# Optimization experiments

Measured on AMD Instinct MI355X. Metric: run time of the kernel, lower is better.

## Reference

```python
import jax, jax.numpy as jnp
import numpy as np

T, B, D = 256, 16, 512          # time, batch, intermediate_dim (GRU is seq-first)
HR = 256                         # router_dim
EXPERT_DIMS = [0, 128, 256, 512]
NUM_TASKS = 4
COST_EXP = 1.0
BN_EPS = 1e-5


def _gru(x, w_ih, w_hh, b_ih, b_hh):
    """PyTorch-semantics GRU over axis 0. x: (T, ..., D) -> (T, ..., H).
    Works batched (T,B,D) or unbatched (N,D) exactly like nn.GRU."""
    H = w_hh.shape[1]
    gi = x @ w_ih.T + b_ih            # (T, ..., 3H) input projections, done once
    h0 = jnp.zeros(x.shape[1:-1] + (H,), x.dtype)

    def step(h, gi_t):
        gh = h @ w_hh.T + b_hh
        i_r, i_z, i_n = jnp.split(gi_t, 3, axis=-1)
        h_r, h_z, h_n = jnp.split(gh, 3, axis=-1)
        r = jax.nn.sigmoid(i_r + h_r)
        z = jax.nn.sigmoid(i_z + h_z)
        n = jnp.tanh(i_n + r * h_n)
        h_new = (1.0 - z) * n + z * h
        return h_new, h_new

    _, ys = jax.lax.scan(step, h0, gi)
    return ys


def setup_inputs() -> dict:
    key = jax.random.key(0)
    ks = iter(jax.random.split(key, 64))

    def p(shape, fan_in):
        return (jax.random.normal(next(ks), shape, jnp.float32) / np.sqrt(fan_in)).astype(jnp.float32)

    inp = {
        'x': jax.random.normal(next(ks), (T, B, D), jnp.float32),
        'task_ids': jax.random.randint(next(ks), (T, B), 0, NUM_TASKS),
        # router params
        'router_w_ih': p((3 * HR, D), D),
        'router_w_hh': p((3 * HR, HR), HR),
        'router_b_ih': jnp.zeros((3 * HR,), jnp.float32),
        'router_b_hh': jnp.zeros((3 * HR,), jnp.float32),
        'router_out_w': p((len(EXPERT_DIMS), HR), HR),
        'router_out_b': jnp.zeros((len(EXPERT_DIMS),), jnp.float32),
    }
    for i, H in enumerate(EXPERT_DIMS):
        if H == 0:
            continue
        inp[f'e{i}_w_ih'] = p((3 * H, D), D)
        inp[f'e{i}_w_hh'] = p((3 * H, H), H)
        inp[f'e{i}_b_ih'] = jnp.zeros((3 * H,), jnp.float32)
        inp[f'e{i}_b_hh'] = jnp.zeros((3 * H,), jnp.float32)
        inp[f'e{i}_bn_g'] = jnp.ones((H,), jnp.float32)
        inp[f'e{i}_bn_b'] = jnp.zeros((H,), jnp.float32)
        inp[f'e{i}_out_w'] = p((D, H), H)
        inp[f'e{i}_out_b'] = jnp.zeros((D,), jnp.float32)
    return inp


def reference(x, task_ids,
              router_w_ih, router_w_hh, router_b_ih, router_b_hh,
              router_out_w, router_out_b,
              e1_w_ih, e1_w_hh, e1_b_ih, e1_b_hh, e1_bn_g, e1_bn_b, e1_out_w, e1_out_b,
              e2_w_ih, e2_w_hh, e2_b_ih, e2_b_hh, e2_bn_g, e2_bn_b, e2_out_w, e2_out_b,
              e3_w_ih, e3_w_hh, e3_b_ih, e3_b_hh, e3_bn_g, e3_bn_b, e3_out_w, e3_out_b):
    E = len(EXPERT_DIMS)
    # ---- router: GRU -> ReLU -> Linear -> softmax ----
    hs = _gru(x, router_w_ih, router_w_hh, router_b_ih, router_b_hh)   # (T,B,HR)
    logits = jax.nn.relu(hs) @ router_out_w.T + router_out_b           # (T,B,E)
    raw = jax.nn.softmax(logits, axis=-1)                              # raw_router_output
    # no dropout configured -> router_output == raw, all experts active

    # ---- task expert usage losses ----
    costs = jnp.asarray([d ** COST_EXP for d in EXPERT_DIMS], logits.dtype)
    eul = jnp.einsum('tbe,e->tb', raw, costs).reshape(-1)
    tflat = task_ids.reshape(-1)
    sums = jax.ops.segment_sum(eul, tflat, num_segments=NUM_TASKS)
    cnts = jax.ops.segment_sum(jnp.ones_like(eul), tflat, num_segments=NUM_TASKS)
    task_losses = sums / cnts                                           # (NUM_TASKS,)

    # ---- experts: each sees the flat (N,D) tokens as ONE unbatched GRU sequence ----
    flat_x = x.reshape(-1, D)                                           # (N,D)
    gates = raw.reshape(-1, E)                                          # (N,E)
    out = gates[:, 0:1] * flat_x                                        # expert 0 = identity

    eps = [(e1_w_ih, e1_w_hh, e1_b_ih, e1_b_hh, e1_bn_g, e1_bn_b, e1_out_w, e1_out_b),
           (e2_w_ih, e2_w_hh, e2_b_ih, e2_b_hh, e2_bn_g, e2_bn_b, e2_out_w, e2_out_b),
           (e3_w_ih, e3_w_hh, e3_b_ih, e3_b_hh, e3_bn_g, e3_bn_b, e3_out_w, e3_out_b)]
    for i, (w_ih, w_hh, b_ih, b_hh, g, b, ow, ob) in enumerate(eps, start=1):
        h = _gru(flat_x, w_ih, w_hh, b_ih, b_hh)                        # (N,H) unbatched seq
        mu = h.mean(0)
        var = ((h - mu) ** 2).mean(0)                                   # biased var (train-mode BN)
        hn = (h - mu) / jnp.sqrt(var + BN_EPS) * g + b
        eo = jax.nn.relu(hn) @ ow.T + ob                                # (N,D)
        out = out + gates[:, i:i + 1] * eo

    final_output = out.reshape(T, B, D)
    return final_output, raw, task_losses
```

## Files before the change

kernel.cpp:

```cpp
#include <hip/hip_runtime.h>
#include <math.h>

constexpr int TT = 256, BB = 16, DD = 512;
constexpr int NTOK = 4096;
constexpr int RTOT = 3456;
constexpr int E1OFF = 768, E2OFF = 1152, E3OFF = 1920;

constexpr size_t OFF_TSUM = 0;
constexpr size_t OFF_TCNT = 16;
constexpr size_t OFF_CNT  = 32;
constexpr size_t ZBYTES   = 64;
constexpr size_t OFF_GI   = 4096;
constexpr size_t OFF_HS   = OFF_GI  + (size_t)NTOK*RTOT*4;
constexpr size_t OFF_HA3  = OFF_HS  + (size_t)NTOK*256*4;
constexpr size_t OFF_HA2  = OFF_HA3 + (size_t)NTOK*512*4;
constexpr size_t OFF_HA1  = OFF_HA2 + (size_t)NTOK*256*4;
constexpr size_t OFF_AP   = OFF_HA1 + (size_t)NTOK*128*4;
constexpr size_t OFF_MU   = OFF_AP  + (size_t)NTOK*896*4;
constexpr size_t OFF_RSTD = OFF_MU  + 896*4;
constexpr size_t POISON_BYTES = (size_t)NTOK*(256+512+256+128)*4;

__device__ __forceinline__ bool is_poison(float v) {
  return __float_as_uint(v) == 0xAAAAAAAAu;
}

__global__ __launch_bounds__(256) void gemm1_kernel(
    const float* __restrict__ X,
    const float* __restrict__ wR, const float* __restrict__ w1,
    const float* __restrict__ w2, const float* __restrict__ w3,
    const float* __restrict__ bR, const float* __restrict__ b1,
    const float* __restrict__ b2, const float* __restrict__ b3,
    float* __restrict__ GI)
{
  __shared__ float At[32*64];
  __shared__ float Bt[32*64];
  const int n0 = blockIdx.x * 64;
  const int r0 = blockIdx.y * 64;
  const float* W; const float* bias; int rs;
  if (r0 < 768)       { W = wR; bias = bR; rs = 0; }
  else if (r0 < 1152) { W = w1; bias = b1; rs = 768; }
  else if (r0 < 1920) { W = w2; bias = b2; rs = 1152; }
  else                { W = w3; bias = b3; rs = 1920; }
  const int lr0 = r0 - rs;
  const int tid = threadIdx.x;
  const int lm = tid & 63, lk4 = tid >> 6;
  const int tx = tid & 15, ty = tid >> 4;
  float acc[4][4];
#pragma unroll
  for (int i = 0; i < 4; ++i)
#pragma unroll
    for (int q = 0; q < 4; ++q) acc[i][q] = 0.f;

  for (int kb = 0; kb < 512; kb += 32) {
    const float4 a0 = *(const float4*)(X + (size_t)(n0+lm)*512 + kb + lk4*8);
    const float4 a1 = *(const float4*)(X + (size_t)(n0+lm)*512 + kb + lk4*8 + 4);
    const float4 c0 = *(const float4*)(W + (size_t)(lr0+lm)*512 + kb + lk4*8);
    const float4 c1 = *(const float4*)(W + (size_t)(lr0+lm)*512 + kb + lk4*8 + 4);
    __syncthreads();
    At[(lk4*8+0)*64+lm]=a0.x; At[(lk4*8+1)*64+lm]=a0.y; At[(lk4*8+2)*64+lm]=a0.z; At[(lk4*8+3)*64+lm]=a0.w;
    At[(lk4*8+4)*64+lm]=a1.x; At[(lk4*8+5)*64+lm]=a1.y; At[(lk4*8+6)*64+lm]=a1.z; At[(lk4*8+7)*64+lm]=a1.w;
    Bt[(lk4*8+0)*64+lm]=c0.x; Bt[(lk4*8+1)*64+lm]=c0.y; Bt[(lk4*8+2)*64+lm]=c0.z; Bt[(lk4*8+3)*64+lm]=c0.w;
    Bt[(lk4*8+4)*64+lm]=c1.x; Bt[(lk4*8+5)*64+lm]=c1.y; Bt[(lk4*8+6)*64+lm]=c1.z; Bt[(lk4*8+7)*64+lm]=c1.w;
    __syncthreads();
#pragma unroll
    for (int k = 0; k < 32; ++k) {
      const float4 av = *(const float4*)&At[k*64 + ty*4];
      const float4 bv = *(const float4*)&Bt[k*64 + tx*4];
      acc[0][0]=fmaf(av.x,bv.x,acc[0][0]); acc[0][1]=fmaf(av.x,bv.y,acc[0][1]); acc[0][2]=fmaf(av.x,bv.z,acc[0][2]); acc[0][3]=fmaf(av.x,bv.w,acc[0][3]);
      acc[1][0]=fmaf(av.y,bv.x,acc[1][0]); acc[1][1]=fmaf(av.y,bv.y,acc[1][1]); acc[1][2]=fmaf(av.y,bv.z,acc[1][2]); acc[1][3]=fmaf(av.y,bv.w,acc[1][3]);
      acc[2][0]=fmaf(av.z,bv.x,acc[2][0]); acc[2][1]=fmaf(av.z,bv.y,acc[2][1]); acc[2][2]=fmaf(av.z,bv.z,acc[2][2]); acc[2][3]=fmaf(av.z,bv.w,acc[2][3]);
      acc[3][0]=fmaf(av.w,bv.x,acc[3][0]); acc[3][1]=fmaf(av.w,bv.y,acc[3][1]); acc[3][2]=fmaf(av.w,bv.z,acc[3][2]); acc[3][3]=fmaf(av.w,bv.w,acc[3][3]);
    }
  }
  const float4 bb = *(const float4*)(bias + lr0 + tx*4);
#pragma unroll
  for (int i = 0; i < 4; ++i) {
    float4 o;
    o.x = acc[i][0] + bb.x; o.y = acc[i][1] + bb.y; o.z = acc[i][2] + bb.z; o.w = acc[i][3] + bb.w;
    *(float4*)(GI + (size_t)(n0+ty*4+i)*RTOT + r0 + tx*4) = o;
  }
}

struct ScanArgs {
  const float* GI;
  const float* rwhh; const float* rbhh; float* hs;
  const float* w1; const float* b1; float* ha1;
  const float* w2; const float* b2; float* ha2;
  const float* w3; const float* b3; float* ha3;
  int* cnt;
};

template<int H, int OPW>
__device__ void expert_scan(const float* __restrict__ GIe, const float* __restrict__ whh,
                            const float* __restrict__ bhh, float* __restrict__ hall,
                            float* __restrict__ sm, int wg)
{
  constexpr int KCN = 512 / OPW;
  constexpr int CHUNK = H / KCN;
  constexpr int NF4 = CHUNK / 4;
  const int tid = threadIdx.x;
  const int j = tid / KCN, kc = tid % KCN;
  const int jg = wg * OPW + j;

  float4 wr[NF4], wz[NF4], wn[NF4];
#pragma unroll
  for (int i4 = 0; i4 < NF4; ++i4) {
    const int kk = kc * CHUNK + ((i4 + kc) & (NF4 - 1)) * 4;
    wr[i4] = *(const float4*)(whh + (size_t)jg * H + kk);
    wz[i4] = *(const float4*)(whh + (size_t)(H + jg) * H + kk);
    wn[i4] = *(const float4*)(whh + (size_t)(2*H + jg) * H + kk);
  }
  float gbr = 0.f, gbz = 0.f, gbn = 0.f;
  float gr0 = 0.f, gz0 = 0.f, gn0 = 0.f, gr1 = 0.f, gz1 = 0.f, gn1 = 0.f;
  if (kc == 0) {
    gbr = bhh[jg]; gbz = bhh[H + jg]; gbn = bhh[2*H + jg];
    gr0 = GIe[jg]; gz0 = GIe[H + jg]; gn0 = GIe[2*H + jg];
    const float* g1 = GIe + RTOT;
    gr1 = g1[jg]; gz1 = g1[H + jg]; gn1 = g1[2*H + jg];
  }
  for (int t = 0; t < NTOK; ++t) {
    float val = 0.f;
    if (tid < H && t > 0) {
      const volatile float* p = (const volatile float*)(hall + (size_t)(t - 1) * H + tid);
      val = *p;
      while (is_poison(val)) val = *p;
    }
    __syncthreads();
    if (tid < H) sm[tid] = val;
    __syncthreads();
    float gr2 = 0.f, gz2 = 0.f, gn2 = 0.f;
    if (kc == 0 && t + 2 < NTOK) {
      const float* g = GIe + (size_t)(t + 2) * RTOT;
      gr2 = g[jg]; gz2 = g[H + jg]; gn2 = g[2*H + jg];
    }
    float pr = 0.f, pz = 0.f, pn = 0.f;
#pragma unroll
    for (int i4 = 0; i4 < NF4; ++i4) {
      const float4 h4 = *(const float4*)(sm + kc * CHUNK + ((i4 + kc) & (NF4 - 1)) * 4);
      pr = fmaf(wr[i4].x, h4.x, pr); pr = fmaf(wr[i4].y, h4.y, pr);
      pr = fmaf(wr[i4].z, h4.z, pr); pr = fmaf(wr[i4].w, h4.w, pr);
      pz = fmaf(wz[i4].x, h4.x, pz); pz = fmaf(wz[i4].y, h4.y, pz);
      pz = fmaf(wz[i4].z, h4.z, pz); pz = fmaf(wz[i4].w, h4.w, pz);
      pn = fmaf(wn[i4].x, h4.x, pn); pn = fmaf(wn[i4].y, h4.y, pn);
      pn = fmaf(wn[i4].z, h4.z, pn); pn = fmaf(wn[i4].w, h4.w, pn);
    }
#pragma unroll
    for (int off = KCN / 2; off; off >>= 1) {
      pr += __shfl_down(pr, off); pz += __shfl_down(pz, off); pn += __shfl_down(pn, off);
    }
    if (kc == 0) {
      const float hprev = sm[jg];
      const float rg = 1.f / (1.f + expf(-(gr0 + gbr + pr)));
      const float zg = 1.f / (1.f + expf(-(gz0 + gbz + pz)));
      const float nn = tanhf(gn0 + rg * (pn + gbn));
      const float hn = (1.f - zg) * nn + zg * hprev;
      *(volatile float*)(hall + (size_t)t * H + jg) = hn;
    }
    gr0 = gr1; gz0 = gz1; gn0 = gn1;
    gr1 = gr2; gz1 = gz2; gn1 = gn2;
  }
}

__device__ void router_scan(const float* __restrict__ GI, const float* __restrict__ whh,
                            const float* __restrict__ bhh, float* __restrict__ hs,
                            float* __restrict__ sm, int wg)
{
  float* hsmB = sm;
  float* pbuf = sm + 16 * 260;
  const int tid = threadIdx.x;
  const int j = tid >> 4, kc = tid & 15;
  const int jg = wg * 32 + j;
  float4 wr4[4], wz4[4], wn4[4];
#pragma unroll
  for (int i4 = 0; i4 < 4; ++i4) {
    const int kk = kc * 16 + ((i4 + kc) & 3) * 4;
    wr4[i4] = *(const float4*)(whh + (size_t)jg * 256 + kk);
    wz4[i4] = *(const float4*)(whh + (size_t)(256 + jg) * 256 + kk);
    wn4[i4] = *(const float4*)(whh + (size_t)(512 + jg) * 256 + kk);
  }
  const int b2 = tid >> 5, j2 = tid & 31;
  const int jg2 = wg * 32 + j2;
  const float gbr = bhh[jg2], gbz = bhh[256 + jg2], gbn = bhh[512 + jg2];
  float gr0, gz0, gn0, gr1, gz1, gn1;
  { const float* g = GI + (size_t)b2 * RTOT;        gr0 = g[jg2]; gz0 = g[256 + jg2]; gn0 = g[512 + jg2]; }
  { const float* g = GI + (size_t)(16 + b2) * RTOT; gr1 = g[jg2]; gz1 = g[256 + jg2]; gn1 = g[512 + jg2]; }
  const int pb = tid >> 5, pk = (tid & 31) * 8;

  for (int t = 0; t < TT; ++t) {
    float gr2 = 0.f, gz2 = 0.f, gn2 = 0.f;
    if (t + 2 < TT) {
      const float* g = GI + (size_t)((t + 2) * 16 + b2) * RTOT;
      gr2 = g[jg2]; gz2 = g[256 + jg2]; gn2 = g[512 + jg2];
    }
    float v[8];
    if (t == 0) {
#pragma unroll
      for (int u = 0; u < 8; ++u) v[u] = 0.f;
    } else {
      const volatile float* q = (const volatile float*)(hs + (size_t)(t - 1) * 4096 + tid * 8);
#pragma unroll
      for (int u = 0; u < 8; ++u) v[u] = q[u];
      bool bad = true;
      while (bad) {
        bad = false;
#pragma unroll
        for (int u = 0; u < 8; ++u)
          if (is_poison(v[u])) { v[u] = q[u]; bad = true; }
      }
    }
    __syncthreads();
    *(float4*)(hsmB + pb * 260 + pk)     = make_float4(v[0], v[1], v[2], v[3]);
    *(float4*)(hsmB + pb * 260 + pk + 4) = make_float4(v[4], v[5], v[6], v[7]);
    __syncthreads();
    float ar[16], az[16], an[16];
#pragma unroll
    for (int b = 0; b < 16; ++b) { ar[b] = 0.f; az[b] = 0.f; an[b] = 0.f; }
#pragma unroll
    for (int i4 = 0; i4 < 4; ++i4) {
      const int col = kc * 16 + ((i4 + kc) & 3) * 4;
#pragma unroll
      for (int b = 0; b < 16; ++b) {
        const float4 h4 = *(const float4*)(hsmB + b * 260 + col);
        ar[b] = fmaf(wr4[i4].x, h4.x, ar[b]); ar[b] = fmaf(wr4[i4].y, h4.y, ar[b]);
        ar[b] = fmaf(wr4[i4].z, h4.z, ar[b]); ar[b] = fmaf(wr4[i4].w, h4.w, ar[b]);
        az[b] = fmaf(wz4[i4].x, h4.x, az[b]); az[b] = fmaf(wz4[i4].y, h4.y, az[b]);
        az[b] = fmaf(wz4[i4].z, h4.z, az[b]); az[b] = fmaf(wz4[i4].w, h4.w, az[b]);
        an[b] = fmaf(wn4[i4].x, h4.x, an[b]); an[b] = fmaf(wn4[i4].y, h4.y, an[b]);
        an[b] = fmaf(wn4[i4].w, h4.w, an[b]); an[b] = fmaf(wn4[i4].z, h4.z, an[b]);
      }
    }
#pragma unroll
    for (int off = 8; off; off >>= 1) {
#pragma unroll
      for (int b = 0; b < 16; ++b) {
        ar[b] += __shfl_down(ar[b], off);
        az[b] += __shfl_down(az[b], off);
        an[b] += __shfl_down(an[b], off);
      }
    }
    if (kc == 0) {
#pragma unroll
      for (int b = 0; b < 16; ++b) {
        pbuf[(b * 32 + j) * 3 + 0] = ar[b];
        pbuf[(b * 32 + j) * 3 + 1] = az[b];
        pbuf[(b * 32 + j) * 3 + 2] = an[b];
      }
    }
    __syncthreads();
    const float pr = pbuf[(b2 * 32 + j2) * 3 + 0];
    const float pz = pbuf[(b2 * 32 + j2) * 3 + 1];
    const float pn = pbuf[(b2 * 32 + j2) * 3 + 2];
    const float hprev = hsmB[b2 * 260 + jg2];
    const float rg = 1.f / (1.f + expf(-(gr0 + gbr + pr)));
    const float zg = 1.f / (1.f + expf(-(gz0 + gbz + pz)));
    const float nn = tanhf(gn0 + rg * (pn + gbn));
    const float hn = (1.f - zg) * nn + zg * hprev;
    *(volatile float*)(hs + (size_t)t * 4096 + b2 * 256 + jg2) = hn;
    gr0 = gr1; gz0 = gz1; gn0 = gn1;
    gr1 = gr2; gz1 = gz2; gn1 = gn2;
  }
}

__global__ __launch_bounds__(512, 1) void scan_kernel(ScanArgs A)
{
  __shared__ float sm[16 * 260 + 1536];
  __shared__ int role_s[2];
  if (threadIdx.x == 0) {
    unsigned x;
    asm volatile("s_getreg_b32 %0, hwreg(HW_REG_XCC_ID)" : "=s"(x));
    const int xcd = (int)(x & 7u);
    role_s[0] = xcd;
    role_s[1] = atomicAdd(A.cnt + xcd, 1);
  }
  __syncthreads();
  const int xcd = role_s[0], r = role_s[1];
  if (xcd == 0)      { if (r < 32) expert_scan<512, 16>(A.GI + E3OFF, A.w3, A.b3, A.ha3, sm, r); }
  else if (xcd == 1) { if (r < 8)  router_scan(A.GI, A.rwhh, A.rbhh, A.hs, sm, r); }
  else if (xcd == 2) { if (r < 16) expert_scan<256, 16>(A.GI + E2OFF, A.w2, A.b2, A.ha2, sm, r); }
  else if (xcd == 3) { if (r < 4)  expert_scan<128, 32>(A.GI + E1OFF, A.w1, A.b1, A.ha1, sm, r); }
}

__global__ __launch_bounds__(256) void router_out_kernel(
    const float* __restrict__ hs, const float* __restrict__ ow, const float* __restrict__ ob,
    const int* __restrict__ tids, float* __restrict__ raw_out,
    float* __restrict__ tsum, float* __restrict__ tcnt)
{
  const int tid = threadIdx.x;
  const int lane = tid & 63, w = tid >> 6;
  const int n = blockIdx.x * 4 + w;
  float s0 = 0.f, s1 = 0.f, s2 = 0.f, s3 = 0.f;
#pragma unroll
  for (int q = 0; q < 4; ++q) {
    const int jj = lane + q * 64;
    float h = hs[(size_t)n * 256 + jj];
    h = h > 0.f ? h : 0.f;
    s0 = fmaf(h, ow[jj], s0);
    s1 = fmaf(h, ow[256 + jj], s1);
    s2 = fmaf(h, ow[512 + jj], s2);
    s3 = fmaf(h, ow[768 + jj], s3);
  }
  for (int off = 32; off; off >>= 1) {
    s0 += __shfl_xor(s0, off); s1 += __shfl_xor(s1, off);
    s2 += __shfl_xor(s2, off); s3 += __shfl_xor(s3, off);
  }
  if (lane == 0) {
    const float l0 = s0 + ob[0], l1 = s1 + ob[1], l2 = s2 + ob[2], l3 = s3 + ob[3];
    const float m = fmaxf(fmaxf(l0, l1), fmaxf(l2, l3));
    const float e0 = expf(l0 - m), e1 = expf(l1 - m), e2 = expf(l2 - m), e3 = expf(l3 - m);
    const float inv = 1.f / (e0 + e1 + e2 + e3);
    float4 rv; rv.x = e0 * inv; rv.y = e1 * inv; rv.z = e2 * inv; rv.w = e3 * inv;
    *(float4*)(raw_out + (size_t)n * 4) = rv;
    const float eul = rv.y * 128.f + rv.z * 256.f + rv.w * 512.f;
    const int tk = tids[n];
    atomicAdd(&tsum[tk], eul);
    atomicAdd(&tcnt[tk], 1.f);
  }
}

__global__ __launch_bounds__(256) void bn_stats_kernel(
    const float* __restrict__ h1, const float* __restrict__ h2, const float* __restrict__ h3,
    float* __restrict__ mu, float* __restrict__ rstd)
{
  const int c = blockIdx.x;
  const float* hp; int He, hc;
  if (c < 128)      { hp = h1; He = 128; hc = c; }
  else if (c < 384) { hp = h2; He = 256; hc = c - 128; }
  else              { hp = h3; He = 512; hc = c - 384; }
  float s = 0.f, s2 = 0.f;
  for (int r = threadIdx.x; r < NTOK; r += 256) {
    const float v = hp[(size_t)r * He + hc];
    s += v; s2 = fmaf(v, v, s2);
  }
  for (int off = 32; off; off >>= 1) { s += __shfl_xor(s, off); s2 += __shfl_xor(s2, off); }
  __shared__ float red[8];
  const int lane = threadIdx.x & 63, w = threadIdx.x >> 6;
  if (lane == 0) { red[w] = s; red[4 + w] = s2; }
  __syncthreads();
  if (threadIdx.x == 0) {
    const float S = red[0] + red[1] + red[2] + red[3];
    const float S2 = red[4] + red[5] + red[6] + red[7];
    const float m = S * (1.f / 4096.f);
    float v = S2 * (1.f / 4096.f) - m * m;
    v = v > 0.f ? v : 0.f;
    mu[c] = m;
    rstd[c] = 1.f / sqrtf(v + 1e-5f);
  }
}

__global__ __launch_bounds__(256) void aprime_kernel(
    const float* __restrict__ h1, const float* __restrict__ h2, const float* __restrict__ h3,
    const float* __restrict__ g1, const float* __restrict__ be1,
    const float* __restrict__ g2, const float* __restrict__ be2,
    const float* __restrict__ g3, const float* __restrict__ be3,
    const float* __restrict__ mu, const float* __restrict__ rstd,
    const float* __restrict__ raw, float* __restrict__ Ap,
    const float* __restrict__ tsum, const float* __restrict__ tcnt, float* __restrict__ tl_out)
{
  if (blockIdx.x == 4096) {
    if (threadIdx.x < 4) tl_out[threadIdx.x] = tsum[threadIdx.x] / tcnt[threadIdx.x];
    return;
  }
  const int n = blockIdx.x;
  for (int c = threadIdx.x; c < 896; c += 256) {
    const float* hp; const float* gg; const float* bb; int He, hc, e;
    if (c < 128)      { hp = h1; gg = g1; bb = be1; He = 128; hc = c;       e = 1; }
    else if (c < 384) { hp = h2; gg = g2; bb = be2; He = 256; hc = c - 128; e = 2; }
    else              { hp = h3; gg = g3; bb = be3; He = 512; hc = c - 384; e = 3; }
    const float h = hp[(size_t)n * He + hc];
    float v = (h - mu[c]) * rstd[c] * gg[hc] + bb[hc];
    v = v > 0.f ? v : 0.f;
    Ap[(size_t)n * 896 + c] = raw[(size_t)n * 4 + e] * v;
  }
}

__global__ __launch_bounds__(256) void out_gemm_kernel(
    const float* __restrict__ Ap,
    const float* __restrict__ ow1, const float* __restrict__ ow2, const float* __restrict__ ow3,
    const float* __restrict__ ob1, const float* __restrict__ ob2, const float* __restrict__ ob3,
    const float* __restrict__ X, const float* __restrict__ raw, float* __restrict__ out)
{
  __shared__ float At[32*64];
  __shared__ float Bt[32*64];
  const int n0 = blockIdx.x * 64;
  const int d0 = blockIdx.y * 64;
  const int tid = threadIdx.x;
  const int lm = tid & 63, lk4 = tid >> 6;
  const int tx = tid & 15, ty = tid >> 4;
  float acc[4][4];
#pragma unroll
  for (int i = 0; i < 4; ++i)
#pragma unroll
    for (int q = 0; q < 4; ++q) acc[i][q] = 0.f;

  for (int kb = 0; kb < 896; kb += 32) {
    const float* W; int He, ko;
    if (kb < 128)      { W = ow1; He = 128; ko = 0; }
    else if (kb < 384) { W = ow2; He = 256; ko = 128; }
    else               { W = ow3; He = 512; ko = 384; }
    const float4 a0 = *(const float4*)(Ap + (size_t)(n0+lm)*896 + kb + lk4*8);
    const float4 a1 = *(const float4*)(Ap + (size_t)(n0+lm)*896 + kb + lk4*8 + 4);
    const float4 c0 = *(const float4*)(W + (size_t)(d0+lm)*He + (kb - ko) + lk4*8);
    const float4 c1 = *(const float4*)(W + (size_t)(d0+lm)*He + (kb - ko) + lk4*8 + 4);
    __syncthreads();
    At[(lk4*8+0)*64+lm]=a0.x; At[(lk4*8+1)*64+lm]=a0.y; At[(lk4*8+2)*64+lm]=a0.z; At[(lk4*8+3)*64+lm]=a0.w;
    At[(lk4*8+4)*64+lm]=a1.x; At[(lk4*8+5)*64+lm]=a1.y; At[(lk4*8+6)*64+lm]=a1.z; At[(lk4*8+7)*64+lm]=a1.w;
    Bt[(lk4*8+0)*64+lm]=c0.x; Bt[(lk4*8+1)*64+lm]=c0.y; Bt[(lk4*8+2)*64+lm]=c0.z; Bt[(lk4*8+3)*64+lm]=c0.w;
    Bt[(lk4*8+4)*64+lm]=c1.x; Bt[(lk4*8+5)*64+lm]=c1.y; Bt[(lk4*8+6)*64+lm]=c1.z; Bt[(lk4*8+7)*64+lm]=c1.w;
    __syncthreads();
#pragma unroll
    for (int k = 0; k < 32; ++k) {
      const float4 av = *(const float4*)&At[k*64 + ty*4];
      const float4 bv = *(const float4*)&Bt[k*64 + tx*4];
      acc[0][0]=fmaf(av.x,bv.x,acc[0][0]); acc[0][1]=fmaf(av.x,bv.y,acc[0][1]); acc[0][2]=fmaf(av.x,bv.z,acc[0][2]); acc[0][3]=fmaf(av.x,bv.w,acc[0][3]);
      acc[1][0]=fmaf(av.y,bv.x,acc[1][0]); acc[1][1]=fmaf(av.y,bv.y,acc[1][1]); acc[1][2]=fmaf(av.y,bv.z,acc[1][2]); acc[1][3]=fmaf(av.y,bv.w,acc[1][3]);
      acc[2][0]=fmaf(av.z,bv.x,acc[2][0]); acc[2][1]=fmaf(av.z,bv.y,acc[2][1]); acc[2][2]=fmaf(av.z,bv.z,acc[2][2]); acc[2][3]=fmaf(av.z,bv.w,acc[2][3]);
      acc[3][0]=fmaf(av.w,bv.x,acc[3][0]); acc[3][1]=fmaf(av.w,bv.y,acc[3][1]); acc[3][2]=fmaf(av.w,bv.z,acc[3][2]); acc[3][3]=fmaf(av.w,bv.w,acc[3][3]);
    }
  }
#pragma unroll
  for (int i = 0; i < 4; ++i) {
    const int n = n0 + ty * 4 + i;
    const float4 g  = *(const float4*)(raw + (size_t)n * 4);
    const float4 xv = *(const float4*)(X + (size_t)n * 512 + d0 + tx * 4);
    const float4 o1 = *(const float4*)(ob1 + d0 + tx * 4);
    const float4 o2 = *(const float4*)(ob2 + d0 + tx * 4);
    const float4 o3 = *(const float4*)(ob3 + d0 + tx * 4);
    float4 o;
    o.x = acc[i][0] + g.x*xv.x + g.y*o1.x + g.z*o2.x + g.w*o3.x;
    o.y = acc[i][1] + g.x*xv.y + g.y*o1.y + g.z*o2.y + g.w*o3.y;
    o.z = acc[i][2] + g.x*xv.z + g.y*o1.z + g.z*o2.z + g.w*o3.z;
    o.w = acc[i][3] + g.x*xv.w + g.y*o1.w + g.z*o2.w + g.w*o3.w;
    *(float4*)(out + (size_t)n * 512 + d0 + tx * 4) = o;
  }
}

extern "C" void kernel_launch(void* const* d_in, const int* in_sizes, int n_in,
                              void* d_out, int out_size, void* d_ws, size_t ws_size,
                              hipStream_t stream) {
  const float* x    = (const float*)d_in[0];
  const int*   tids = (const int*)d_in[1];
  const float* rwih = (const float*)d_in[2];
  const float* rwhh = (const float*)d_in[3];
  const float* rbih = (const float*)d_in[4];
  const float* rbhh = (const float*)d_in[5];
  const float* row  = (const float*)d_in[6];
  const float* rob  = (const float*)d_in[7];
  const float* w1ih = (const float*)d_in[8];
  const float* w1hh = (const float*)d_in[9];
  const float* b1ih = (const float*)d_in[10];
  const float* b1hh = (const float*)d_in[11];
  const float* bn1g = (const float*)d_in[12];
  const float* bn1b = (const float*)d_in[13];
  const float* ow1  = (const float*)d_in[14];
  const float* ob1  = (const float*)d_in[15];
  const float* w2ih = (const float*)d_in[16];
  const float* w2hh = (const float*)d_in[17];
  const float* b2ih = (const float*)d_in[18];
  const float* b2hh = (const float*)d_in[19];
  const float* bn2g = (const float*)d_in[20];
  const float* bn2b = (const float*)d_in[21];
  const float* ow2  = (const float*)d_in[22];
  const float* ob2  = (const float*)d_in[23];
  const float* w3ih = (const float*)d_in[24];
  const float* w3hh = (const float*)d_in[25];
  const float* b3ih = (const float*)d_in[26];
  const float* b3hh = (const float*)d_in[27];
  const float* bn3g = (const float*)d_in[28];
  const float* bn3b = (const float*)d_in[29];
  const float* ow3  = (const float*)d_in[30];
  const float* ob3  = (const float*)d_in[31];

  char* ws = (char*)d_ws;
  float* tsum = (float*)(ws + OFF_TSUM);
  float* tcnt = (float*)(ws + OFF_TCNT);
  int*   cnt  = (int*)(ws + OFF_CNT);
  float* GI   = (float*)(ws + OFF_GI);
  float* hs   = (float*)(ws + OFF_HS);
  float* ha3  = (float*)(ws + OFF_HA3);
  float* ha2  = (float*)(ws + OFF_HA2);
  float* ha1  = (float*)(ws + OFF_HA1);
  float* Ap   = (float*)(ws + OFF_AP);
  float* mu   = (float*)(ws + OFF_MU);
  float* rstd = (float*)(ws + OFF_RSTD);

  float* outp = (float*)d_out;
  float* rawp = outp + (size_t)NTOK * DD;
  float* tlp  = rawp + (size_t)NTOK * 4;

  hipMemsetAsync(ws, 0, ZBYTES, stream);
  hipMemsetAsync(ws + OFF_HS, 0xAA, POISON_BYTES, stream);

  gemm1_kernel<<<dim3(64, 54), 256, 0, stream>>>(x, rwih, w1ih, w2ih, w3ih,
                                                 rbih, b1ih, b2ih, b3ih, GI);

  ScanArgs sa;
  sa.GI = GI; sa.rwhh = rwhh; sa.rbhh = rbhh; sa.hs = hs;
  sa.w1 = w1hh; sa.b1 = b1hh; sa.ha1 = ha1;
  sa.w2 = w2hh; sa.b2 = b2hh; sa.ha2 = ha2;
  sa.w3 = w3hh; sa.b3 = b3hh; sa.ha3 = ha3;
  sa.cnt = cnt;
  scan_kernel<<<dim3(320), dim3(512), 0, stream>>>(sa);

  router_out_kernel<<<dim3(1024), 256, 0, stream>>>(hs, row, rob, tids, rawp, tsum, tcnt);
  bn_stats_kernel<<<dim3(896), 256, 0, stream>>>(ha1, ha2, ha3, mu, rstd);
  aprime_kernel<<<dim3(4097), 256, 0, stream>>>(ha1, ha2, ha3, bn1g, bn1b, bn2g, bn2b,
                                                bn3g, bn3b, mu, rstd, rawp, Ap,
                                                tsum, tcnt, tlp);

  out_gemm_kernel<<<dim3(64, 8), 256, 0, stream>>>(Ap, ow1, ow2, ow3, ob1, ob2, ob3,
                                                   x, rawp, outp);
}
```

Baseline: 7.303 ms.

## Streamline expert GRU scan step: double-buffered h, wide polling, shuffled GI prefetch

Reworks the per-step loop of the cross-workgroup expert GRU scan. The previous hidden state is polled by fewer threads using 64-bit atomic loads and written into a double-buffered shared array, which cuts the step from two barriers to one. The input-gate values for KCN steps ahead are prefetched across the lanes of each reduction group and broadcast with shuffles, replacing per-step global loads on the critical path. hprev is now kept in a register instead of being read from shared memory. The polling now depends on 8-byte aligned poison detection, and the FMA order in the two scans is swapped slightly, which can change rounding.

```diff
diff --git a/kernel.cpp b/kernel.cpp
--- a/kernel.cpp
+++ b/kernel.cpp
@@ -22,6 +22,9 @@
 
 __device__ __forceinline__ bool is_poison(float v) {
   return __float_as_uint(v) == 0xAAAAAAAAu;
+}
+__device__ __forceinline__ bool u64_has_poison(unsigned long long w) {
+  return ((unsigned)w == 0xAAAAAAAAu) || ((unsigned)(w >> 32) == 0xAAAAAAAAu);
 }
 
 __global__ __launch_bounds__(256) void gemm1_kernel(
@@ -101,6 +104,7 @@
   const int tid = threadIdx.x;
   const int j = tid / KCN, kc = tid % KCN;
   const int jg = wg * OPW + j;
+  const int lane = tid & 63;
 
   float4 wr[NF4], wz[NF4], wn[NF4];
 #pragma unroll
@@ -110,54 +114,83 @@
     wz[i4] = *(const float4*)(whh + (size_t)(H + jg) * H + kk);
     wn[i4] = *(const float4*)(whh + (size_t)(2*H + jg) * H + kk);
   }
-  float gbr = 0.f, gbz = 0.f, gbn = 0.f;
-  float gr0 = 0.f, gz0 = 0.f, gn0 = 0.f, gr1 = 0.f, gz1 = 0.f, gn1 = 0.f;
-  if (kc == 0) {
-    gbr = bhh[jg]; gbz = bhh[H + jg]; gbn = bhh[2*H + jg];
-    gr0 = GIe[jg]; gz0 = GIe[H + jg]; gn0 = GIe[2*H + jg];
-    const float* g1 = GIe + RTOT;
-    gr1 = g1[jg]; gz1 = g1[H + jg]; gn1 = g1[2*H + jg];
-  }
+  float gbr = 0.f, gbz = 0.f, gbn = 0.f, hprev = 0.f;
+  if (kc == 0) { gbr = bhh[jg]; gbz = bhh[H + jg]; gbn = bhh[2*H + jg]; }
+
+  float gAr, gAz, gAn, gBr, gBz, gBn;
+  { const float* g = GIe + (size_t)kc * RTOT;
+    gAr = g[jg]; gAz = g[H + jg]; gAn = g[2*H + jg]; }
+  { const float* g = GIe + (size_t)(KCN + kc) * RTOT;
+    gBr = g[jg]; gBz = g[H + jg]; gBn = g[2*H + jg]; }
+
   for (int t = 0; t < NTOK; ++t) {
-    float val = 0.f;
-    if (tid < H && t > 0) {
-      const volatile float* p = (const volatile float*)(hall + (size_t)(t - 1) * H + tid);
-      val = *p;
-      while (is_poison(val)) val = *p;
-    }
-    __syncthreads();
-    if (tid < H) sm[tid] = val;
-    __syncthreads();
-    float gr2 = 0.f, gz2 = 0.f, gn2 = 0.f;
-    if (kc == 0 && t + 2 < NTOK) {
-      const float* g = GIe + (size_t)(t + 2) * RTOT;
-      gr2 = g[jg]; gz2 = g[H + jg]; gn2 = g[2*H + jg];
-    }
+    if (tid < H / 8) {
+      unsigned long long w[4];
+      if (t == 0) {
+#pragma unroll
+        for (int i = 0; i < 4; ++i) w[i] = 0ull;
+      } else {
+        const unsigned long long* p =
+            (const unsigned long long*)(hall + (size_t)(t - 1) * H) + tid * 4;
+#pragma unroll
+        for (int i = 0; i < 4; ++i)
+          w[i] = __hip_atomic_load(p + i, __ATOMIC_RELAXED, __HIP_MEMORY_SCOPE_AGENT);
+        for (;;) {
+          bool bad = false;
+#pragma unroll
+          for (int i = 0; i < 4; ++i)
+            if (u64_has_poison(w[i])) {
+              w[i] = __hip_atomic_load(p + i, __ATOMIC_RELAXED, __HIP_MEMORY_SCOPE_AGENT);
+              bad = true;
+            }
+          if (!bad) break;
+        }
+      }
+      unsigned long long* dst =
+          (unsigned long long*)(sm + (size_t)(t & 1) * H) + tid * 4;
+#pragma unroll
+      for (int i = 0; i < 4; ++i) dst[i] = w[i];
+    }
+    __syncthreads();
+    const float* hbuf = sm + (size_t)(t & 1) * H;
+
+    const int m = t & (KCN - 1);
+    const int src = (lane & ~(KCN - 1)) | m;
+    const float gr0 = __shfl(gAr, src);
+    const float gz0 = __shfl(gAz, src);
+    const float gn0 = __shfl(gAn, src);
+
     float pr = 0.f, pz = 0.f, pn = 0.f;
 #pragma unroll
     for (int i4 = 0; i4 < NF4; ++i4) {
-      const float4 h4 = *(const float4*)(sm + kc * CHUNK + ((i4 + kc) & (NF4 - 1)) * 4);
+      const float4 h4 = *(const float4*)(hbuf + kc * CHUNK + ((i4 + kc) & (NF4 - 1)) * 4);
       pr = fmaf(wr[i4].x, h4.x, pr); pr = fmaf(wr[i4].y, h4.y, pr);
       pr = fmaf(wr[i4].z, h4.z, pr); pr = fmaf(wr[i4].w, h4.w, pr);
       pz = fmaf(wz[i4].x, h4.x, pz); pz = fmaf(wz[i4].y, h4.y, pz);
       pz = fmaf(wz[i4].z, h4.z, pz); pz = fmaf(wz[i4].w, h4.w, pz);
       pn = fmaf(wn[i4].x, h4.x, pn); pn = fmaf(wn[i4].y, h4.y, pn);
-      pn = fmaf(wn[i4].z, h4.z, pn); pn = fmaf(wn[i4].w, h4.w, pn);
+      pn = fmaf(wn[i4].w, h4.w, pn); pn = fmaf(wn[i4].z, h4.z, pn);
     }
 #pragma unroll
     for (int off = KCN / 2; off; off >>= 1) {
       pr += __shfl_down(pr, off); pz += __shfl_down(pz, off); pn += __shfl_down(pn, off);
     }
     if (kc == 0) {
-      const float hprev = sm[jg];
       const float rg = 1.f / (1.f + expf(-(gr0 + gbr + pr)));
       const float zg = 1.f / (1.f + expf(-(gz0 + gbz + pz)));
       const float nn = tanhf(gn0 + rg * (pn + gbn));
       const float hn = (1.f - zg) * nn + zg * hprev;
+      hprev = hn;
       *(volatile float*)(hall + (size_t)t * H + jg) = hn;
     }
-    gr0 = gr1; gz0 = gz1; gn0 = gn1;
-    gr1 = gr2; gz1 = gz2; gn1 = gn2;
+    if (m == KCN - 1) {
+      gAr = gBr; gAz = gBz; gAn = gBn;
+      const int nb = t + 1 + KCN;
+      if (nb + kc < NTOK) {
+        const float* g = GIe + (size_t)(nb + kc) * RTOT;
+        gBr = g[jg]; gBz = g[H + jg]; gBn = g[2*H + jg];
+      }
+    }
   }
 }
 
@@ -226,7 +259,7 @@
         az[b] = fmaf(wz4[i4].x, h4.x, az[b]); az[b] = fmaf(wz4[i4].y, h4.y, az[b]);
         az[b] = fmaf(wz4[i4].z, h4.z, az[b]); az[b] = fmaf(wz4[i4].w, h4.w, az[b]);
         an[b] = fmaf(wn4[i4].x, h4.x, an[b]); an[b] = fmaf(wn4[i4].y, h4.y, an[b]);
-        an[b] = fmaf(wn4[i4].w, h4.w, an[b]); an[b] = fmaf(wn4[i4].z, h4.z, an[b]);
+        an[b] = fmaf(wn4[i4].z, h4.z, an[b]); an[b] = fmaf(wn4[i4].w, h4.w, an[b]);
       }
     }
 #pragma unroll
@@ -263,7 +296,7 @@
 
 __global__ __launch_bounds__(512, 1) void scan_kernel(ScanArgs A)
 {
-  __shared__ float sm[16 * 260 + 1536];
+  __shared__ __attribute__((aligned(16))) float sm[16 * 260 + 1536];
   __shared__ int role_s[2];
   if (threadIdx.x == 0) {
     unsigned x;
```

Result: slower. 8.879 ms (+21.6%).
